# Kernel optimization log

Measured on AMD Instinct MI355X. Metric: run time of the kernel, lower is better.

## Reference

```python
import jax, jax.numpy as jnp
import numpy as np


def _apply_ry(state, c, s, wire):
    """Apply RY with cos/sin of theta/2 (c, s broadcastable over batch) on `wire`.
    PennyLane wire 0 is the most-significant qubit.
    state: [B, 2**Q] real float32."""
    B, N = state.shape
    st = state.reshape(B, 2 ** wire, 2, -1)
    a, b = st[:, :, 0], st[:, :, 1]
    st = jnp.stack([c * a - s * b, s * a + c * b], axis=2)
    return st.reshape(B, N)


def _apply_cnot_chain_step(state, ctrl):
    """CNOT with control=ctrl, target=ctrl+1 (adjacent wires)."""
    B, N = state.shape
    st = state.reshape(B, 2 ** ctrl, 2, 2, -1)
    st = jnp.stack([st[:, :, 0], st[:, :, 1, ::-1]], axis=2)
    return st.reshape(B, N)


def setup_inputs() -> dict:
    key = jax.random.key(0)
    k1, k2 = jax.random.split(key)
    B, Q, L = 512, 14, 2
    x = jax.random.normal(k1, (B, Q), dtype=jnp.float32)          # encoding angles
    weights = 0.5 * jax.random.normal(k2, (L, Q), dtype=jnp.float32)  # nn.Parameter randn*0.5
    return {"x": x, "weights": weights}


def reference(x, weights):
    B, Q = x.shape
    L = weights.shape[0]
    N_OUT = Q  # n_outputs == n_qubits here

    # |0...0> initial state, real-valued (RY and CNOT are real matrices)
    state = jnp.zeros((B, 2 ** Q), dtype=x.dtype).at[:, 0].set(1.0)

    # Angle encoding: RY(x_i) on wire i (per-sample angles)
    for i in range(Q):
        half = 0.5 * x[:, i]
        state = _apply_ry(state, jnp.cos(half)[:, None, None], jnp.sin(half)[:, None, None], i)

    # Variational layers: RY(weights[l, i]) per qubit, then CNOT ladder
    for l in range(L):
        for i in range(Q):
            half = 0.5 * weights[l, i]
            state = _apply_ry(state, jnp.cos(half), jnp.sin(half), i)
        for i in range(Q - 1):
            state = _apply_cnot_chain_step(state, i)

    # <Z_i> = P(wire i = 0) - P(wire i = 1)
    probs = state * state  # [B, 2**Q]
    outs = []
    for i in range(N_OUT):
        p = probs.reshape(B, 2 ** i, 2, -1).sum(axis=(1, 3))  # [B, 2]
        outs.append(p[:, 0] - p[:, 1])
    return jnp.stack(outs, axis=1).astype(jnp.float32)  # [B, n_outputs]
```

## Files before the change

### kernel.cpp

```cpp
#include <hip/hip_runtime.h>
#include <math.h>


#define Q 14

__global__ __launch_bounds__(64)
void quantum_kernel(const float* __restrict__ x,
                    const float* __restrict__ w,
                    float* __restrict__ out,
                    int B)
{
    const int b = blockIdx.x * 64 + threadIdx.x;
    if (b >= B) return;

    float ca[Q], sa[Q], s2a[Q], cw[Q], sw[Q];
#pragma unroll
    for (int j = 0; j < Q; ++j) {
        float alpha = 0.5f * (x[b * Q + j] + w[j]);
        float s, c;
        sincosf(alpha, &s, &c);
        ca[j] = c;
        sa[j] = s;
        s2a[j] = 2.0f * c * s;
        sincosf(w[Q + j], &sw[j], &cw[j]);
    }

    float f00 = 1.0f, f11 = 0.0f, f01 = 0.0f;
#pragma unroll
    for (int j = 0; j < Q; ++j) {
        const float c = ca[j], s = sa[j];
        const float cc = c * c, ss = s * s, cs = c * s;
        const float cross = 2.0f * cs * f01;
        const float h00 = cc * f00 + cross + ss * f11;
        const float h11 = ss * f00 + cross + cc * f11;
        const float h01 = cs * (f00 + f11) + f01;
        f00 = cw[j] * h00;
        f11 = -cw[j] * h11;
        f01 = -sw[j] * h01;
        const float g = (j < Q - 1) ? s2a[j + 1] : 1.0f;
        out[b * Q + j] = f00 + f11 + 2.0f * g * f01;
    }
}

extern "C" void kernel_launch(void* const* d_in, const int* in_sizes, int n_in,
                              void* d_out, int out_size, void* d_ws, size_t ws_size,
                              hipStream_t stream) {
    const float* x = (const float*)d_in[0];
    const float* w = (const float*)d_in[1];
    float* out = (float*)d_out;
    const int B = in_sizes[0] / Q;
    const int grid = (B + 63) / 64;
    quantum_kernel<<<dim3(grid), dim3(64), 0, stream>>>(x, w, out, B);
}
```

Before: 57.85 us.

## Parallelize per-qubit trig across threads via shared memory, then serial recurrence

Splits the work so that each (row, qubit) pair's sincos is computed by its own thread and stored in shared memory, instead of one thread doing all 28 sincos for its sample. Each block now handles 16 rows with 256 threads, giving 32 blocks in total. A subset of 16 threads then runs the serial 14-step recurrence from shared memory. The goal is to shorten per-thread latency from the sequential sincos calls. The costs are a barrier, only 16 of 256 threads active in the second phase, and fewer total blocks.

```diff
diff --git a/kernel.cpp b/kernel.cpp
--- a/kernel.cpp
+++ b/kernel.cpp
@@ -3,42 +3,65 @@
 
 
 #define Q 14
+#define ROWS 16
+#define BLOCK 256
 
-__global__ __launch_bounds__(64)
+__global__ __launch_bounds__(BLOCK)
 void quantum_kernel(const float* __restrict__ x,
                     const float* __restrict__ w,
                     float* __restrict__ out,
                     int B)
 {
-    const int b = blockIdx.x * 64 + threadIdx.x;
-    if (b >= B) return;
+    __shared__ float2 csA[ROWS][Q];
+    __shared__ float  s2A[ROWS][Q];
+    __shared__ float2 csW[Q];
 
-    float ca[Q], sa[Q], s2a[Q], cw[Q], sw[Q];
+    const int t = threadIdx.x;
+    const int rowBase = blockIdx.x * ROWS;
+
+    if (t < ROWS * Q) {
+        const int r = t / Q;
+        const int j = t - r * Q;
+        const int b = rowBase + r;
+        if (b < B) {
+            const float alpha = 0.5f * (x[b * Q + j] + w[j]);
+            float s, c;
+            sincosf(alpha, &s, &c);
+            csA[r][j] = make_float2(c, s);
+            s2A[r][j] = 2.0f * c * s;
+        }
+        if (r == 0) {
+            float sw_, cw_;
+            sincosf(w[Q + j], &sw_, &cw_);
+            csW[j] = make_float2(cw_, sw_);
+        }
+    }
+    __syncthreads();
+
+    if (t < ROWS) {
+        const int b = rowBase + t;
+        if (b < B) {
+            float f00 = 1.0f, f11 = 0.0f, f01 = 0.0f;
+            float outv[Q];
 #pragma unroll
-    for (int j = 0; j < Q; ++j) {
-        float alpha = 0.5f * (x[b * Q + j] + w[j]);
-        float s, c;
-        sincosf(alpha, &s, &c);
-        ca[j] = c;
-        sa[j] = s;
-        s2a[j] = 2.0f * c * s;
-        sincosf(w[Q + j], &sw[j], &cw[j]);
-    }
-
-    float f00 = 1.0f, f11 = 0.0f, f01 = 0.0f;
+            for (int j = 0; j < Q; ++j) {
+                const float2 cs = csA[t][j];
+                const float c = cs.x, s = cs.y;
+                const float cc = c * c, ss = s * s, csx = c * s;
+                const float cross = 2.0f * csx * f01;
+                const float h00 = cc * f00 + cross + ss * f11;
+                const float h11 = ss * f00 + cross + cc * f11;
+                const float h01 = csx * (f00 + f11) + f01;
+                const float2 wv = csW[j];
+                f00 =  wv.x * h00;
+                f11 = -wv.x * h11;
+                f01 = -wv.y * h01;
+                const float g = (j < Q - 1) ? s2A[t][j + 1] : 1.0f;
+                outv[j] = f00 + f11 + 2.0f * g * f01;
+            }
 #pragma unroll
-    for (int j = 0; j < Q; ++j) {
-        const float c = ca[j], s = sa[j];
-        const float cc = c * c, ss = s * s, cs = c * s;
-        const float cross = 2.0f * cs * f01;
-        const float h00 = cc * f00 + cross + ss * f11;
-        const float h11 = ss * f00 + cross + cc * f11;
-        const float h01 = cs * (f00 + f11) + f01;
-        f00 = cw[j] * h00;
-        f11 = -cw[j] * h11;
-        f01 = -sw[j] * h01;
-        const float g = (j < Q - 1) ? s2a[j + 1] : 1.0f;
-        out[b * Q + j] = f00 + f11 + 2.0f * g * f01;
+            for (int j = 0; j < Q; ++j) out[b * Q + j] = outv[j];
+        }
     }
 }
 
@@ -49,6 +72,6 @@
     const float* w = (const float*)d_in[1];
     float* out = (float*)d_out;
     const int B = in_sizes[0] / Q;
-    const int grid = (B + 63) / 64;
-    quantum_kernel<<<dim3(grid), dim3(64), 0, stream>>>(x, w, out, B);
+    const int grid = (B + ROWS - 1) / ROWS;
+    quantum_kernel<<<dim3(grid), dim3(BLOCK), 0, stream>>>(x, w, out, B);
 }
```

Result: faster. 55.49 us (-4.1%).
